# Performance work log

Hardware: AMD Instinct MI355X
Metric: run time of the kernel (lower is better)

Reference implementation:

```python
import jax, jax.numpy as jnp
import numpy as np

D_MODEL = 1024
MAX_LEN = 2048
BATCH = 4


def _causal_mask(max_len):
    # tril ones -> 0 on/below diag, -inf above (added to scores BEFORE scaling,
    # matching the original module's order of operations)
    return jnp.where(jnp.tril(jnp.ones((max_len, max_len), dtype=bool)), 0.0, -jnp.inf).astype(jnp.float32)


def setup_inputs() -> dict:
    key = jax.random.key(0)
    ks = jax.random.split(key, 9)
    s = 1.0 / np.sqrt(D_MODEL)  # torch Linear default init scale (uniform bound)
    return {
        "encoded_q": jax.random.normal(ks[0], (BATCH, MAX_LEN, D_MODEL), jnp.float32),
        "encoded_k": jax.random.normal(ks[1], (BATCH, MAX_LEN, D_MODEL), jnp.float32),
        "encoded_v": jax.random.normal(ks[2], (BATCH, MAX_LEN, D_MODEL), jnp.float32),
        "W_q": jax.random.uniform(ks[3], (D_MODEL, D_MODEL), jnp.float32, -s, s),
        "b_q": jax.random.uniform(ks[4], (D_MODEL,), jnp.float32, -s, s),
        "W_k": jax.random.uniform(ks[5], (D_MODEL, D_MODEL), jnp.float32, -s, s),
        "b_k": jax.random.uniform(ks[6], (D_MODEL,), jnp.float32, -s, s),
        "W_v": jax.random.uniform(ks[7], (D_MODEL, D_MODEL), jnp.float32, -s, s),
        "b_v": jax.random.uniform(ks[8], (D_MODEL,), jnp.float32, -s, s),
        "parameter_mask": 1,
    }


def reference(encoded_q, encoded_k, encoded_v, W_q, b_q, W_k, b_k, W_v, b_v, parameter_mask):
    # torch Linear: y = x @ W.T + b
    q = jnp.einsum("bsd,ed->bse", encoded_q, W_q) + b_q  # [B,S,D]
    k = jnp.einsum("bsd,ed->bse", encoded_k, W_k) + b_k
    v = jnp.einsum("bsd,ed->bse", encoded_v, W_v) + b_v
    values = jnp.einsum("bqd,bkd->bqk", q, k)  # [B,S,S]
    if parameter_mask:
        values = values + _causal_mask(values.shape[-1])
    scaled = values / jnp.sqrt(jnp.float32(D_MODEL))
    attn = jax.nn.softmax(scaled, axis=-1)
    return jnp.einsum("bqk,bkd->bqd", attn, v)  # [B,S,D]
```

## Files before the change

kernel.cpp:

```cpp
#include <hip/hip_runtime.h>

typedef __bf16 bf16;
typedef __attribute__((ext_vector_type(8))) __bf16 bf16x8;
typedef __attribute__((ext_vector_type(4))) __bf16 bf16x4;
typedef __attribute__((ext_vector_type(4))) float f32x4;

#define S_LEN 2048
#define DM 1024
#define NB 4

__device__ __forceinline__ void async_copy16(const void* g, void* l)
{
    __builtin_amdgcn_global_load_lds(
        (const __attribute__((address_space(1))) unsigned int*)g,
        (__attribute__((address_space(3))) unsigned int*)l,
        16, 0, 0);
}

#define VM_WAIT8 asm volatile("s_waitcnt vmcnt(8)" ::: "memory")
#define VM_WAIT0 asm volatile("s_waitcnt vmcnt(0)" ::: "memory")
#define LGKM0    asm volatile("s_waitcnt lgkmcnt(0)" ::: "memory")
#define BAR      asm volatile("s_barrier" ::: "memory")


__device__ __forceinline__ void stage_issue(const char* aGk, size_t aRow32,
                                            const char* bGk, size_t bRow32,
                                            char* aL, char* bL)
{
#pragma unroll
    for (int i = 0; i < 4; i++) {
        async_copy16(aGk + i * aRow32, aL + i * 4096);
        async_copy16(bGk + i * bRow32, bL + i * 4096);
    }
}

__device__ __forceinline__ void read_frags(const char* bufA, const char* bufB,
                                           int wr, int wc, int l16, int quad,
                                           bf16x8 (&af)[2][4], bf16x8 (&bfr)[2][4])
{
    const int swz = l16 & 7;
#pragma unroll
    for (int kk = 0; kk < 2; kk++) {
        const int col = (((kk << 2) + quad) ^ swz) << 4;
#pragma unroll
        for (int t = 0; t < 4; t++) {
            af[kk][t]  = *(const bf16x8*)(bufA + (wr * 64 + t * 16 + l16) * 128 + col);
            bfr[kk][t] = *(const bf16x8*)(bufB + (wc * 64 + t * 16 + l16) * 128 + col);
        }
    }
}

__device__ __forceinline__ void mfma_all(const bf16x8 (&af)[2][4],
                                         const bf16x8 (&bfr)[2][4],
                                         f32x4 (&acc)[4][4])
{
#pragma unroll
    for (int kk = 0; kk < 2; kk++)
#pragma unroll
        for (int rt = 0; rt < 4; rt++)
#pragma unroll
            for (int ct = 0; ct < 4; ct++)
                acc[rt][ct] = __builtin_amdgcn_mfma_f32_16x16x32_bf16(
                    af[kk][rt], bfr[kk][ct], acc[rt][ct], 0, 0, 0);
}

__device__ __forceinline__ void gemm_tile(
    const bf16* __restrict__ A, int lda,
    const bf16* __restrict__ B, int ldb,
    int kSteps, char* smem, f32x4 (&acc)[4][4])
{
    const int tid = threadIdx.x;
    const int w = tid >> 6, lane = tid & 63;
    const int quad = lane >> 4, l16 = lane & 15;
    const int wr = w >> 1, wc = w & 1;

#pragma unroll
    for (int i = 0; i < 4; i++)
#pragma unroll
        for (int j = 0; j < 4; j++) acc[i][j] = f32x4{0.f, 0.f, 0.f, 0.f};

    const int srow = tid >> 3;
    const int sc8  = tid & 7;
    const int srcCol = (sc8 ^ (srow & 7)) * 16;
    const char* aG = (const char*)(A + (size_t)srow * lda) + srcCol;
    const char* bG = (const char*)(B + (size_t)srow * ldb) + srcCol;
    const size_t aRow32 = (size_t)lda * 64;
    const size_t bRow32 = (size_t)ldb * 64;
    char* aL0 = smem +     0 + w * 1024;
    char* bL0 = smem + 16384 + w * 1024;
    char* aL1 = smem + 32768 + w * 1024;
    char* bL1 = smem + 49152 + w * 1024;

    stage_issue(aG,       aRow32, bG,       bRow32, aL0, bL0);
    stage_issue(aG + 128, aRow32, bG + 128, bRow32, aL1, bL1);

    for (int ks = 0; ks < kSteps; ks += 2) {
        const bool more = (ks + 2 < kSteps);
        bf16x8 af[2][4], bfr[2][4];

        VM_WAIT8;
        BAR;
        read_frags(smem, smem + 16384, wr, wc, l16, quad, af, bfr);
        LGKM0;
        BAR;
        if (more)
            stage_issue(aG + (size_t)(ks + 2) * 128, aRow32,
                        bG + (size_t)(ks + 2) * 128, bRow32, aL0, bL0);
        mfma_all(af, bfr, acc);

        if (more) { VM_WAIT8; } else { VM_WAIT0; }
        BAR;
        read_frags(smem + 32768, smem + 49152, wr, wc, l16, quad, af, bfr);
        LGKM0;
        BAR;
        if (more)
            stage_issue(aG + (size_t)(ks + 3) * 128, aRow32,
                        bG + (size_t)(ks + 3) * 128, bRow32, aL1, bL1);
        mfma_all(af, bfr, acc);
    }
}

__global__ __launch_bounds__(256) void cvt3_kernel(
    const float* __restrict__ s0, const float* __restrict__ s1, const float* __restrict__ s2,
    bf16* __restrict__ d0, bf16* __restrict__ d1, bf16* __restrict__ d2)
{
    const float* src = blockIdx.y == 0 ? s0 : blockIdx.y == 1 ? s1 : s2;
    bf16* dst        = blockIdx.y == 0 ? d0 : blockIdx.y == 1 ? d1 : d2;
    size_t i = ((size_t)blockIdx.x * 256 + threadIdx.x) * 8;
    f32x4 a = *(const f32x4*)(src + i);
    f32x4 b = *(const f32x4*)(src + i + 4);
    bf16x8 o;
    o[0] = (bf16)a[0]; o[1] = (bf16)a[1]; o[2] = (bf16)a[2]; o[3] = (bf16)a[3];
    o[4] = (bf16)b[0]; o[5] = (bf16)b[1]; o[6] = (bf16)b[2]; o[7] = (bf16)b[3];
    *(bf16x8*)(dst + i) = o;
}

__global__ __launch_bounds__(256) void projqk_kernel(
    const bf16* __restrict__ Eq, const bf16* __restrict__ Ek,
    const bf16* __restrict__ Wq, const bf16* __restrict__ Wk,
    const float* __restrict__ bq, const float* __restrict__ bk,
    bf16* __restrict__ Qo, bf16* __restrict__ Ko)
{
    __shared__ __align__(16) char smem[65536];
    const int bid = blockIdx.x;
    const int c = bid & 7;
    const int j = bid >> 3;
    const int z = j >> 6;
    const int r64 = j & 63;
    const int m0 = (c * 8 + (r64 >> 3)) * 128;
    const int n0 = (r64 & 7) * 128;

    const bf16* E     = z == 0 ? Eq : Ek;
    const bf16* W     = z == 0 ? Wq : Wk;
    const float* bias = z == 0 ? bq : bk;

    f32x4 acc[4][4];
    gemm_tile(E + (size_t)m0 * DM, DM, W + (size_t)n0 * DM, DM, DM / 64, smem, acc);

    const int tid = threadIdx.x;
    const int w = tid >> 6, lane = tid & 63;
    const int quad = lane >> 4, l16 = lane & 15;
    const int wr = w >> 1, wc = w & 1;
    const int nBase = n0 + wc * 64;

    float bcol[4];
#pragma unroll
    for (int ct = 0; ct < 4; ct++) bcol[ct] = bias[nBase + ct * 16 + l16];

    __syncthreads();
    bf16* Tt = (bf16*)smem;
#pragma unroll
    for (int rt = 0; rt < 4; rt++)
#pragma unroll
        for (int ct = 0; ct < 4; ct++)
#pragma unroll
            for (int r = 0; r < 4; r++)
                Tt[(wr * 64 + rt * 16 + quad * 4 + r) * 136 + wc * 64 + ct * 16 + l16]
                    = (bf16)(acc[rt][ct][r] + bcol[ct]);
    __syncthreads();
    bf16* O = z == 0 ? Qo : Ko;
    const int row = tid >> 1, half = tid & 1;
    const bf16* src = Tt + row * 136 + half * 64;
    bf16* dst = O + (size_t)(m0 + row) * DM + n0 + half * 64;
#pragma unroll
    for (int i = 0; i < 8; i++)
        *(bf16x8*)(dst + i * 8) = *(const bf16x8*)(src + i * 8);
}

__global__ __launch_bounds__(256) void projv_qk_kernel(
    const bf16* __restrict__ Ev, const bf16* __restrict__ Wv,
    const float* __restrict__ bv, bf16* __restrict__ Vt,
    const bf16* __restrict__ Q, const bf16* __restrict__ K,
    const int* __restrict__ maskp, bf16* __restrict__ P, float* __restrict__ lsum)
{
    __shared__ __align__(16) char smem[65536];
    const int bid = blockIdx.x;
    const int tid = threadIdx.x;
    const int w = tid >> 6, lane = tid & 63;
    const int quad = lane >> 4, l16 = lane & 15;
    const int wr = w >> 1, wc = w & 1;

    if (bid < 512) {
        const int c = bid & 7;
        const int r64 = bid >> 3;
        const int m0 = (c * 8 + (r64 >> 3)) * 128;
        const int n0 = (r64 & 7) * 128;

        f32x4 acc[4][4];
        gemm_tile(Ev + (size_t)m0 * DM, DM, Wv + (size_t)n0 * DM, DM, DM / 64, smem, acc);

        const int nBase = n0 + wc * 64;
        float bcol[4];
#pragma unroll
        for (int ct = 0; ct < 4; ct++) bcol[ct] = bv[nBase + ct * 16 + l16];

        const int mBase = m0 + wr * 64;
#pragma unroll
        for (int rt = 0; rt < 4; rt++) {
            const int m = mBase + rt * 16 + quad * 4;
            const int bb = m >> 11;
            const int s  = m & 2047;
#pragma unroll
            for (int ct = 0; ct < 4; ct++) {
                const int n = nBase + ct * 16 + l16;
                bf16x4 o;
                o[0] = (bf16)(acc[rt][ct][0] + bcol[ct]);
                o[1] = (bf16)(acc[rt][ct][1] + bcol[ct]);
                o[2] = (bf16)(acc[rt][ct][2] + bcol[ct]);
                o[3] = (bf16)(acc[rt][ct][3] + bcol[ct]);
                *(bf16x4*)(Vt + ((size_t)(bb * DM + n)) * S_LEN + s) = o;
            }
        }
    } else {
        const int qbid = bid - 512;
        const int c = qbid & 7;
        const int j = qbid >> 3;
        const int b = j >> 5;
        const int jj = j & 31;
        const int kt = (jj < 16) ? c : (15 - c);
        const int qt = jj & 15;
        const bool causal = (maskp[0] != 0);
        if (causal && kt > qt) return;

        f32x4 acc[4][4];
        const bf16* Qb = Q + ((size_t)(b * S_LEN + qt * 128)) * DM;
        const bf16* Kb = K + ((size_t)(b * S_LEN + kt * 128)) * DM;
        gemm_tile(Qb, DM, Kb, DM, DM / 64, smem, acc);

        const float scale = 0.03125f;

        __syncthreads();
        bf16* Pt = (bf16*)smem;
#pragma unroll
        for (int rt = 0; rt < 4; rt++)
#pragma unroll
            for (int r = 0; r < 4; r++) {
                const int rloc = wr * 64 + rt * 16 + quad * 4 + r;
                const int qg = qt * 128 + rloc;
#pragma unroll
                for (int ct = 0; ct < 4; ct++) {
                    const int kg = kt * 128 + wc * 64 + ct * 16 + l16;
                    float p = (!causal || kg <= qg) ? __expf(acc[rt][ct][r] * scale) : 0.0f;
                    Pt[rloc * 136 + wc * 64 + ct * 16 + l16] = (bf16)p;
                }
            }
        __syncthreads();

        bf16* Pb = P + (size_t)b * S_LEN * S_LEN;
        float* lb = lsum + b * S_LEN;
        const int row = tid >> 1, half = tid & 1;
        const bf16* src = Pt + row * 136 + half * 64;
        bf16* dst = Pb + (size_t)(qt * 128 + row) * S_LEN + kt * 128 + half * 64;
        float rs = 0.0f;
#pragma unroll
        for (int i = 0; i < 8; i++) {
            bf16x8 x = *(const bf16x8*)(src + i * 8);
            *(bf16x8*)(dst + i * 8) = x;
#pragma unroll
            for (int e = 0; e < 8; e++) rs += (float)x[e];
        }
        rs += __shfl_xor(rs, 1);
        if (half == 0) atomicAdd(&lb[qt * 128 + row], rs);
    }
}

__global__ __launch_bounds__(256) void pv_kernel(
    const bf16* __restrict__ P, const bf16* __restrict__ Vt,
    const float* __restrict__ lsum, const int* __restrict__ maskp,
    float* __restrict__ Out)
{
    const int bid = blockIdx.x;
    const int c = bid & 7;
    const int b = c >> 1;
    const int par = c & 1;
    const int idx = bid >> 3;
    const int dt = idx & 7;
    const int qi = idx >> 3;
    const int qt = (7 - qi) * 2 + par;
    const bool causal = (maskp[0] != 0);
    const int kSteps = causal ? (qt + 1) * 2 : (S_LEN / 64);

    __shared__ __align__(16) char smem[65536];

    f32x4 acc[4][4];
    const bf16* Pb = P + ((size_t)b * S_LEN + qt * 128) * S_LEN;
    const bf16* Vb = Vt + ((size_t)(b * DM + dt * 128)) * S_LEN;
    gemm_tile(Pb, S_LEN, Vb, S_LEN, kSteps, smem, acc);

    const int tid = threadIdx.x;
    const int w = tid >> 6, lane = tid & 63;
    const int quad = lane >> 4, l16 = lane & 15;
    const int wr = w >> 1, wc = w & 1;

    const float* lb = lsum + b * S_LEN;
    float inv[4][4];
#pragma unroll
    for (int rt = 0; rt < 4; rt++)
#pragma unroll
        for (int r = 0; r < 4; r++)
            inv[rt][r] = 1.0f / lb[qt * 128 + wr * 64 + rt * 16 + quad * 4 + r];

    __syncthreads();
    float* Ot = (float*)smem;
#pragma unroll
    for (int h = 0; h < 2; h++) {
        if (wr == h) {
#pragma unroll
            for (int rt = 0; rt < 4; rt++)
#pragma unroll
                for (int r = 0; r < 4; r++) {
                    const int rloc = rt * 16 + quad * 4 + r;
#pragma unroll
                    for (int ct = 0; ct < 4; ct++)
                        Ot[rloc * 132 + wc * 64 + ct * 16 + l16] = acc[rt][ct][r] * inv[rt][r];
                }
        }
        __syncthreads();
        const int row = tid >> 2, qq = tid & 3;
        const float* src = Ot + row * 132 + qq * 32;
        float* dst = Out + (size_t)(b * S_LEN + qt * 128 + h * 64 + row) * DM + dt * 128 + qq * 32;
#pragma unroll
        for (int i = 0; i < 8; i++)
            *(f32x4*)(dst + i * 4) = *(const f32x4*)(src + i * 4);
        __syncthreads();
    }
}

extern "C" void kernel_launch(void* const* d_in, const int* in_sizes, int n_in,
                              void* d_out, int out_size, void* d_ws, size_t ws_size,
                              hipStream_t stream)
{
    const float* Eq = (const float*)d_in[0];
    const float* Ek = (const float*)d_in[1];
    const float* Ev = (const float*)d_in[2];
    const float* Wq = (const float*)d_in[3];
    const float* bq = (const float*)d_in[4];
    const float* Wk = (const float*)d_in[5];
    const float* bk = (const float*)d_in[6];
    const float* Wv = (const float*)d_in[7];
    const float* bv = (const float*)d_in[8];
    const int* maskp = (const int*)d_in[9];
    float* Out = (float*)d_out;

    char* ws = (char*)d_ws;
    const size_t SZ_QKV = (size_t)NB * S_LEN * DM * 2;
    const size_t SZ_W   = (size_t)DM * DM * 2;
    bf16* Qb  = (bf16*)(ws);
    bf16* Kb  = (bf16*)(ws + SZ_QKV);
    bf16* Vtb = (bf16*)(ws + 2 * SZ_QKV);
    bf16* Wqb = (bf16*)(ws + 3 * SZ_QKV);
    bf16* Wkb = (bf16*)(ws + 3 * SZ_QKV + SZ_W);
    bf16* Wvb = (bf16*)(ws + 3 * SZ_QKV + 2 * SZ_W);
    float* lsum = (float*)(ws + 3 * SZ_QKV + 3 * SZ_W);
    bf16* Pbuf = (bf16*)(ws + 3 * SZ_QKV + 3 * SZ_W + (1 << 20));
    bf16* Eqb = Pbuf;
    bf16* Ekb = Eqb + (size_t)NB * S_LEN * DM;
    bf16* Evb = Ekb + (size_t)NB * S_LEN * DM;

    hipMemsetAsync(lsum, 0, (size_t)NB * S_LEN * 4, stream);
    cvt3_kernel<<<dim3(512, 3), 256, 0, stream>>>(Wq, Wk, Wv, Wqb, Wkb, Wvb);
    cvt3_kernel<<<dim3(4096, 3), 256, 0, stream>>>(Eq, Ek, Ev, Eqb, Ekb, Evb);

    projqk_kernel<<<1024, 256, 0, stream>>>(
        Eqb, Ekb, Wqb, Wkb, bq, bk, Qb, Kb);

    projv_qk_kernel<<<1536, 256, 0, stream>>>(
        Evb, Wvb, bv, Vtb, Qb, Kb, maskp, Pbuf, lsum);

    pv_kernel<<<512, 256, 0, stream>>>(Pbuf, Vtb, lsum, maskp, Out);
}
```

Measured before the change: 280.9 us.

## Fuse fp32-to-bf16 conversion into projection GEMM loads and drop cvt kernels

The separate cvt3 kernels and the memset are removed. The projection GEMMs now read fp32 inputs and weights directly, convert to bf16 in registers and write the result to LDS through a register-staged pipeline. Extra blocks in the projection kernel zero lsum, and the fused kernel now schedules the QK^T blocks before the V projection. The pv_kernel q-tile ordering is also reshuffled for load balance. This saves a full fp32 read plus bf16 write pass, but it gives up async global-to-LDS copies and doubles the global bytes read per GEMM tile.

```diff
diff --git a/kernel.cpp b/kernel.cpp
--- a/kernel.cpp
+++ b/kernel.cpp
@@ -23,6 +23,37 @@
 #define BAR      asm volatile("s_barrier" ::: "memory")
 
 
+__device__ __forceinline__ void read_frags(const char* bufA, const char* bufB,
+                                           int wr, int wc, int l16, int quad,
+                                           bf16x8 (&af)[2][4], bf16x8 (&bfr)[2][4])
+{
+    const int swz = l16 & 7;
+#pragma unroll
+    for (int kk = 0; kk < 2; kk++) {
+        const int col = (((kk << 2) + quad) ^ swz) << 4;
+#pragma unroll
+        for (int t = 0; t < 4; t++) {
+            af[kk][t]  = *(const bf16x8*)(bufA + (wr * 64 + t * 16 + l16) * 128 + col);
+            bfr[kk][t] = *(const bf16x8*)(bufB + (wc * 64 + t * 16 + l16) * 128 + col);
+        }
+    }
+}
+
+__device__ __forceinline__ void mfma_all(const bf16x8 (&af)[2][4],
+                                         const bf16x8 (&bfr)[2][4],
+                                         f32x4 (&acc)[4][4])
+{
+#pragma unroll
+    for (int kk = 0; kk < 2; kk++)
+#pragma unroll
+        for (int rt = 0; rt < 4; rt++)
+#pragma unroll
+            for (int ct = 0; ct < 4; ct++)
+                acc[rt][ct] = __builtin_amdgcn_mfma_f32_16x16x32_bf16(
+                    af[kk][rt], bfr[kk][ct], acc[rt][ct], 0, 0, 0);
+}
+
+
 __device__ __forceinline__ void stage_issue(const char* aGk, size_t aRow32,
                                             const char* bGk, size_t bRow32,
                                             char* aL, char* bL)
@@ -32,36 +63,6 @@
         async_copy16(aGk + i * aRow32, aL + i * 4096);
         async_copy16(bGk + i * bRow32, bL + i * 4096);
     }
-}
-
-__device__ __forceinline__ void read_frags(const char* bufA, const char* bufB,
-                                           int wr, int wc, int l16, int quad,
-                                           bf16x8 (&af)[2][4], bf16x8 (&bfr)[2][4])
-{
-    const int swz = l16 & 7;
-#pragma unroll
-    for (int kk = 0; kk < 2; kk++) {
-        const int col = (((kk << 2) + quad) ^ swz) << 4;
-#pragma unroll
-        for (int t = 0; t < 4; t++) {
-            af[kk][t]  = *(const bf16x8*)(bufA + (wr * 64 + t * 16 + l16) * 128 + col);
-            bfr[kk][t] = *(const bf16x8*)(bufB + (wc * 64 + t * 16 + l16) * 128 + col);
-        }
-    }
-}
-
-__device__ __forceinline__ void mfma_all(const bf16x8 (&af)[2][4],
-                                         const bf16x8 (&bfr)[2][4],
-                                         f32x4 (&acc)[4][4])
-{
-#pragma unroll
-    for (int kk = 0; kk < 2; kk++)
-#pragma unroll
-        for (int rt = 0; rt < 4; rt++)
-#pragma unroll
-            for (int ct = 0; ct < 4; ct++)
-                acc[rt][ct] = __builtin_amdgcn_mfma_f32_16x16x32_bf16(
-                    af[kk][rt], bfr[kk][ct], acc[rt][ct], 0, 0, 0);
 }
 
 __device__ __forceinline__ void gemm_tile(
@@ -120,44 +121,117 @@
     }
 }
 
-__global__ __launch_bounds__(256) void cvt3_kernel(
-    const float* __restrict__ s0, const float* __restrict__ s1, const float* __restrict__ s2,
-    bf16* __restrict__ d0, bf16* __restrict__ d1, bf16* __restrict__ d2)
-{
-    const float* src = blockIdx.y == 0 ? s0 : blockIdx.y == 1 ? s1 : s2;
-    bf16* dst        = blockIdx.y == 0 ? d0 : blockIdx.y == 1 ? d1 : d2;
-    size_t i = ((size_t)blockIdx.x * 256 + threadIdx.x) * 8;
-    f32x4 a = *(const f32x4*)(src + i);
-    f32x4 b = *(const f32x4*)(src + i + 4);
-    bf16x8 o;
-    o[0] = (bf16)a[0]; o[1] = (bf16)a[1]; o[2] = (bf16)a[2]; o[3] = (bf16)a[3];
-    o[4] = (bf16)b[0]; o[5] = (bf16)b[1]; o[6] = (bf16)b[2]; o[7] = (bf16)b[3];
-    *(bf16x8*)(dst + i) = o;
-}
-
-__global__ __launch_bounds__(256) void projqk_kernel(
-    const bf16* __restrict__ Eq, const bf16* __restrict__ Ek,
-    const bf16* __restrict__ Wq, const bf16* __restrict__ Wk,
+
+__device__ __forceinline__ void loads_f32(const float* aG, int lda,
+                                          const float* bG, int ldb, int t,
+                                          f32x4 (&sA)[4][2], f32x4 (&sB)[4][2])
+{
+#pragma unroll
+    for (int i = 0; i < 4; i++) {
+        const float* ap = aG + (size_t)i * 32 * lda + t * 64;
+        const float* bp = bG + (size_t)i * 32 * ldb + t * 64;
+        sA[i][0] = *(const f32x4*)(ap);
+        sA[i][1] = *(const f32x4*)(ap + 4);
+        sB[i][0] = *(const f32x4*)(bp);
+        sB[i][1] = *(const f32x4*)(bp + 4);
+    }
+}
+
+__device__ __forceinline__ void cvtwrite(char* aL, char* bL,
+                                         const f32x4 (&sA)[4][2], const f32x4 (&sB)[4][2])
+{
+#pragma unroll
+    for (int i = 0; i < 4; i++) {
+        bf16x8 oa, ob;
+#pragma unroll
+        for (int e = 0; e < 4; e++) {
+            oa[e] = (bf16)sA[i][0][e]; oa[e + 4] = (bf16)sA[i][1][e];
+            ob[e] = (bf16)sB[i][0][e]; ob[e + 4] = (bf16)sB[i][1][e];
+        }
+        *(bf16x8*)(aL + i * 4096) = oa;
+        *(bf16x8*)(bL + i * 4096) = ob;
+    }
+}
+
+__device__ __forceinline__ void gemm_tile_f32(
+    const float* __restrict__ A, int lda,
+    const float* __restrict__ B, int ldb,
+    int kSteps, char* smem, f32x4 (&acc)[4][4])
+{
+    const int tid = threadIdx.x;
+    const int w = tid >> 6, lane = tid & 63;
+    const int quad = lane >> 4, l16 = lane & 15;
+    const int wr = w >> 1, wc = w & 1;
+
+#pragma unroll
+    for (int i = 0; i < 4; i++)
+#pragma unroll
+        for (int j = 0; j < 4; j++) acc[i][j] = f32x4{0.f, 0.f, 0.f, 0.f};
+
+    const int srow = tid >> 3;
+    const int sc8  = tid & 7;
+    const int srcChunk = sc8 ^ (srow & 7);
+    const float* aG = A + (size_t)srow * lda + srcChunk * 8;
+    const float* bG = B + (size_t)srow * ldb + srcChunk * 8;
+    char* aL = smem + tid * 16;
+    char* bL = smem + 16384 + tid * 16;
+
+    f32x4 sA[4][2], sB[4][2];
+    loads_f32(aG, lda, bG, ldb, 0, sA, sB);
+    VM_WAIT0;
+    cvtwrite(aL, bL, sA, sB);
+    loads_f32(aG, lda, bG, ldb, 1, sA, sB);
+    VM_WAIT0;
+    cvtwrite(aL + 32768, bL + 32768, sA, sB);
+    if (kSteps > 2) loads_f32(aG, lda, bG, ldb, 2, sA, sB);
+    LGKM0;
+
+    for (int t = 0; t < kSteps; t++) {
+        const int boff = (t & 1) * 32768;
+        bf16x8 af[2][4], bfr[2][4];
+        BAR;
+        read_frags(smem + boff, smem + boff + 16384, wr, wc, l16, quad, af, bfr);
+        LGKM0;
+        BAR;
+        if (t + 2 < kSteps) {
+            VM_WAIT0;
+            cvtwrite(aL + boff, bL + boff, sA, sB);
+            if (t + 3 < kSteps)
+                loads_f32(aG, lda, bG, ldb, t + 3, sA, sB);
+        }
+        mfma_all(af, bfr, acc);
+    }
+}
+
+__global__ __launch_bounds__(256, 2) void projqk_kernel(
+    const float* __restrict__ Eq, const float* __restrict__ Ek,
+    const float* __restrict__ Wq, const float* __restrict__ Wk,
     const float* __restrict__ bq, const float* __restrict__ bk,
-    bf16* __restrict__ Qo, bf16* __restrict__ Ko)
+    bf16* __restrict__ Qo, bf16* __restrict__ Ko, float* __restrict__ lsum)
 {
     __shared__ __align__(16) char smem[65536];
     const int bid = blockIdx.x;
-    const int c = bid & 7;
-    const int j = bid >> 3;
+    const int tid = threadIdx.x;
+
+    if (bid < 8) {
+        *(f32x4*)(lsum + (bid * 1024) + tid * 4) = f32x4{0.f, 0.f, 0.f, 0.f};
+        return;
+    }
+    const int g = bid - 8;
+    const int c = g & 7;
+    const int j = g >> 3;
     const int z = j >> 6;
     const int r64 = j & 63;
     const int m0 = (c * 8 + (r64 >> 3)) * 128;
     const int n0 = (r64 & 7) * 128;
 
-    const bf16* E     = z == 0 ? Eq : Ek;
-    const bf16* W     = z == 0 ? Wq : Wk;
+    const float* E    = z == 0 ? Eq : Ek;
+    const float* W    = z == 0 ? Wq : Wk;
     const float* bias = z == 0 ? bq : bk;
 
     f32x4 acc[4][4];
-    gemm_tile(E + (size_t)m0 * DM, DM, W + (size_t)n0 * DM, DM, DM / 64, smem, acc);
-
-    const int tid = threadIdx.x;
+    gemm_tile_f32(E + (size_t)m0 * DM, DM, W + (size_t)n0 * DM, DM, DM / 64, smem, acc);
+
     const int w = tid >> 6, lane = tid & 63;
     const int quad = lane >> 4, l16 = lane & 15;
     const int wr = w >> 1, wc = w & 1;
@@ -187,8 +261,8 @@
         *(bf16x8*)(dst + i * 8) = *(const bf16x8*)(src + i * 8);
 }
 
-__global__ __launch_bounds__(256) void projv_qk_kernel(
-    const bf16* __restrict__ Ev, const bf16* __restrict__ Wv,
+__global__ __launch_bounds__(256, 2) void projv_qk_kernel(
+    const float* __restrict__ Ev, const float* __restrict__ Wv,
     const float* __restrict__ bv, bf16* __restrict__ Vt,
     const bf16* __restrict__ Q, const bf16* __restrict__ K,
     const int* __restrict__ maskp, bf16* __restrict__ P, float* __restrict__ lsum)
@@ -200,14 +274,64 @@
     const int quad = lane >> 4, l16 = lane & 15;
     const int wr = w >> 1, wc = w & 1;
 
-    if (bid < 512) {
+    if (bid < 1024) {
         const int c = bid & 7;
-        const int r64 = bid >> 3;
+        const int j = bid >> 3;
+        const int b = j >> 5;
+        const int jj = j & 31;
+        const int kt = (jj < 16) ? c : (15 - c);
+        const int qt = jj & 15;
+        const bool causal = (maskp[0] != 0);
+        if (causal && kt > qt) return;
+
+        f32x4 acc[4][4];
+        const bf16* Qb = Q + ((size_t)(b * S_LEN + qt * 128)) * DM;
+        const bf16* Kb = K + ((size_t)(b * S_LEN + kt * 128)) * DM;
+        gemm_tile(Qb, DM, Kb, DM, DM / 64, smem, acc);
+
+        const float scale = 0.03125f;
+
+        __syncthreads();
+        bf16* Pt = (bf16*)smem;
+#pragma unroll
+        for (int rt = 0; rt < 4; rt++)
+#pragma unroll
+            for (int r = 0; r < 4; r++) {
+                const int rloc = wr * 64 + rt * 16 + quad * 4 + r;
+                const int qg = qt * 128 + rloc;
+#pragma unroll
+                for (int ct = 0; ct < 4; ct++) {
+                    const int kg = kt * 128 + wc * 64 + ct * 16 + l16;
+                    float p = (!causal || kg <= qg) ? __expf(acc[rt][ct][r] * scale) : 0.0f;
+                    Pt[rloc * 136 + wc * 64 + ct * 16 + l16] = (bf16)p;
+                }
+            }
+        __syncthreads();
+
+        bf16* Pb = P + (size_t)b * S_LEN * S_LEN;
+        float* lb = lsum + b * S_LEN;
+        const int row = tid >> 1, half = tid & 1;
+        const bf16* src = Pt + row * 136 + half * 64;
+        bf16* dst = Pb + (size_t)(qt * 128 + row) * S_LEN + kt * 128 + half * 64;
+        float rs = 0.0f;
+#pragma unroll
+        for (int i = 0; i < 8; i++) {
+            bf16x8 x = *(const bf16x8*)(src + i * 8);
+            *(bf16x8*)(dst + i * 8) = x;
+#pragma unroll
+            for (int e = 0; e < 8; e++) rs += (float)x[e];
+        }
+        rs += __shfl_xor(rs, 1);
+        if (half == 0) atomicAdd(&lb[qt * 128 + row], rs);
+    } else {
+        const int vbid = bid - 1024;
+        const int c = vbid & 7;
+        const int r64 = vbid >> 3;
         const int m0 = (c * 8 + (r64 >> 3)) * 128;
         const int n0 = (r64 & 7) * 128;
 
         f32x4 acc[4][4];
-        gemm_tile(Ev + (size_t)m0 * DM, DM, Wv + (size_t)n0 * DM, DM, DM / 64, smem, acc);
+        gemm_tile_f32(Ev + (size_t)m0 * DM, DM, Wv + (size_t)n0 * DM, DM, DM / 64, smem, acc);
 
         const int nBase = n0 + wc * 64;
         float bcol[4];
@@ -231,56 +355,6 @@
                 *(bf16x4*)(Vt + ((size_t)(bb * DM + n)) * S_LEN + s) = o;
             }
         }
-    } else {
-        const int qbid = bid - 512;
-        const int c = qbid & 7;
-        const int j = qbid >> 3;
-        const int b = j >> 5;
-        const int jj = j & 31;
-        const int kt = (jj < 16) ? c : (15 - c);
-        const int qt = jj & 15;
-        const bool causal = (maskp[0] != 0);
-        if (causal && kt > qt) return;
-
-        f32x4 acc[4][4];
-        const bf16* Qb = Q + ((size_t)(b * S_LEN + qt * 128)) * DM;
-        const bf16* Kb = K + ((size_t)(b * S_LEN + kt * 128)) * DM;
-        gemm_tile(Qb, DM, Kb, DM, DM / 64, smem, acc);
-
-        const float scale = 0.03125f;
-
-        __syncthreads();
-        bf16* Pt = (bf16*)smem;
-#pragma unroll
-        for (int rt = 0; rt < 4; rt++)
-#pragma unroll
-            for (int r = 0; r < 4; r++) {
-                const int rloc = wr * 64 + rt * 16 + quad * 4 + r;
-                const int qg = qt * 128 + rloc;
-#pragma unroll
-                for (int ct = 0; ct < 4; ct++) {
-                    const int kg = kt * 128 + wc * 64 + ct * 16 + l16;
-                    float p = (!causal || kg <= qg) ? __expf(acc[rt][ct][r] * scale) : 0.0f;
-                    Pt[rloc * 136 + wc * 64 + ct * 16 + l16] = (bf16)p;
-                }
-            }
-        __syncthreads();
-
-        bf16* Pb = P + (size_t)b * S_LEN * S_LEN;
-        float* lb = lsum + b * S_LEN;
-        const int row = tid >> 1, half = tid & 1;
-        const bf16* src = Pt + row * 136 + half * 64;
-        bf16* dst = Pb + (size_t)(qt * 128 + row) * S_LEN + kt * 128 + half * 64;
-        float rs = 0.0f;
-#pragma unroll
-        for (int i = 0; i < 8; i++) {
-            bf16x8 x = *(const bf16x8*)(src + i * 8);
-            *(bf16x8*)(dst + i * 8) = x;
-#pragma unroll
-            for (int e = 0; e < 8; e++) rs += (float)x[e];
-        }
-        rs += __shfl_xor(rs, 1);
-        if (half == 0) atomicAdd(&lb[qt * 128 + row], rs);
     }
 }
 
@@ -296,7 +370,9 @@
     const int idx = bid >> 3;
     const int dt = idx & 7;
     const int qi = idx >> 3;
-    const int qt = (7 - qi) * 2 + par;
+    const int kk = (qi + dt) & 7;
+    const unsigned tbl = par ? 0x65219ADEu : 0x74308BCFu;
+    const int qt = (tbl >> (kk * 4)) & 15;
     const bool causal = (maskp[0] != 0);
     const int kSteps = causal ? (qt + 1) * 2 : (S_LEN / 64);
 
@@ -364,28 +440,17 @@
 
     char* ws = (char*)d_ws;
     const size_t SZ_QKV = (size_t)NB * S_LEN * DM * 2;
-    const size_t SZ_W   = (size_t)DM * DM * 2;
     bf16* Qb  = (bf16*)(ws);
     bf16* Kb  = (bf16*)(ws + SZ_QKV);
     bf16* Vtb = (bf16*)(ws + 2 * SZ_QKV);
-    bf16* Wqb = (bf16*)(ws + 3 * SZ_QKV);
-    bf16* Wkb = (bf16*)(ws + 3 * SZ_QKV + SZ_W);
-    bf16* Wvb = (bf16*)(ws + 3 * SZ_QKV + 2 * SZ_W);
-    float* lsum = (float*)(ws + 3 * SZ_QKV + 3 * SZ_W);
-    bf16* Pbuf = (bf16*)(ws + 3 * SZ_QKV + 3 * SZ_W + (1 << 20));
-    bf16* Eqb = Pbuf;
-    bf16* Ekb = Eqb + (size_t)NB * S_LEN * DM;
-    bf16* Evb = Ekb + (size_t)NB * S_LEN * DM;
-
-    hipMemsetAsync(lsum, 0, (size_t)NB * S_LEN * 4, stream);
-    cvt3_kernel<<<dim3(512, 3), 256, 0, stream>>>(Wq, Wk, Wv, Wqb, Wkb, Wvb);
-    cvt3_kernel<<<dim3(4096, 3), 256, 0, stream>>>(Eq, Ek, Ev, Eqb, Ekb, Evb);
-
-    projqk_kernel<<<1024, 256, 0, stream>>>(
-        Eqb, Ekb, Wqb, Wkb, bq, bk, Qb, Kb);
+    float* lsum = (float*)(ws + 3 * SZ_QKV);
+    bf16* Pbuf = (bf16*)(ws + 3 * SZ_QKV + (1 << 20));
+
+    projqk_kernel<<<1032, 256, 0, stream>>>(
+        Eq, Ek, Wq, Wk, bq, bk, Qb, Kb, lsum);
 
     projv_qk_kernel<<<1536, 256, 0, stream>>>(
-        Evb, Wvb, bv, Vtb, Qb, Kb, maskp, Pbuf, lsum);
+        Ev, Wv, bv, Vtb, Qb, Kb, maskp, Pbuf, lsum);
 
     pv_kernel<<<512, 256, 0, stream>>>(Pbuf, Vtb, lsum, maskp, Out);
 }
```

Measured after the change: 314.8 us. 1.12x slower.
